# Optimization experiments

Hardware: AMD Instinct MI355X
Metric: run time of the kernel (lower is better)

The kernel has to match this reference:

```python
import jax, jax.numpy as jnp
import numpy as np

B, S, I, H, A = 512, 256, 12, 256, 9


def _lstm_layer(x, w_ih, w_hh, b_ih, b_hh):
    # x: [B,S,in] -> outputs [B,S,H], final (h, c). PyTorch gate order i,f,g,o.
    b, s, _ = x.shape
    h_dim = w_hh.shape[1]
    xg = jnp.einsum('bsi,gi->bsg', x, w_ih) + b_ih  # [B,S,4H] precomputed input gates

    def step(carry, xg_t):
        h, c = carry
        gates = xg_t + h @ w_hh.T + b_hh
        i_g, f_g, g_g, o_g = jnp.split(gates, 4, axis=-1)
        c = jax.nn.sigmoid(f_g) * c + jax.nn.sigmoid(i_g) * jnp.tanh(g_g)
        h = jax.nn.sigmoid(o_g) * jnp.tanh(c)
        return (h, c), h

    init = (jnp.zeros((b, h_dim), x.dtype), jnp.zeros((b, h_dim), x.dtype))
    (h, c), ys = jax.lax.scan(step, init, jnp.swapaxes(xg, 0, 1))
    return jnp.swapaxes(ys, 0, 1), h, c


def setup_inputs() -> dict:
    key = jax.random.key(0)
    ks = jax.random.split(key, 20)
    sc = 0.1
    inp = {
        'x': jax.random.normal(ks[0], (B, S, I), jnp.float32),
        'mask': jnp.ones((B, A), jnp.float32),
        'W_emb': jax.random.normal(ks[1], (H, I), jnp.float32) * sc,
        'b_emb': jnp.zeros((H,), jnp.float32),
        'w_ih0': jax.random.normal(ks[2], (4 * H, H), jnp.float32) * sc,
        'w_hh0': jax.random.normal(ks[3], (4 * H, H), jnp.float32) * sc,
        'b_ih0': jnp.zeros((4 * H,), jnp.float32),
        'b_hh0': jnp.zeros((4 * H,), jnp.float32),
        'w_ih1': jax.random.normal(ks[4], (4 * H, H), jnp.float32) * sc,
        'w_hh1': jax.random.normal(ks[5], (4 * H, H), jnp.float32) * sc,
        'b_ih1': jnp.zeros((4 * H,), jnp.float32),
        'b_hh1': jnp.zeros((4 * H,), jnp.float32),
        'ln_g': jnp.ones((H,), jnp.float32),
        'ln_b': jnp.zeros((H,), jnp.float32),
        'w1': jax.random.normal(ks[6], (32, H), jnp.float32) * sc,
        'b1': jnp.zeros((32,), jnp.float32),
        'w2': jax.random.normal(ks[7], (A, 32), jnp.float32) * sc,
        'b2': jnp.zeros((A,), jnp.float32),
    }
    return inp


def reference(x, mask, W_emb, b_emb, w_ih0, w_hh0, b_ih0, b_hh0,
              w_ih1, w_hh1, b_ih1, b_hh1, ln_g, ln_b, w1, b1, w2, b2):
    # embed + ReLU
    emb = jax.nn.relu(jnp.einsum('bsi,hi->bsh', x, W_emb) + b_emb)  # [B,S,H]
    # 2-layer LSTM (dropout between layers is identity in eval mode)
    y0, h0, c0 = _lstm_layer(emb, w_ih0, w_hh0, b_ih0, b_hh0)
    y1, h1, c1 = _lstm_layer(y0, w_ih1, w_hh1, b_ih1, b_hh1)
    last = y1[:, -1, :]  # [B,H]
    # LayerNorm
    mu = jnp.mean(last, axis=-1, keepdims=True)
    var = jnp.mean((last - mu) ** 2, axis=-1, keepdims=True)
    normed = (last - mu) / jnp.sqrt(var + 1e-5) * ln_g + ln_b
    # MLP head (dropout identity in eval)
    hdn = jax.nn.relu(normed @ w1.T + b1)
    logits = hdn @ w2.T + b2  # [B,A]
    logits = logits + (1.0 - mask) * -1e9
    hidden = (jnp.stack([h0, h1]), jnp.stack([c0, c1]))
    return logits, hidden
```

## Files before the change

### kernel.cpp

```cpp
#include <hip/hip_runtime.h>
#include <cstdint>
#include <cstddef>

typedef __attribute__((ext_vector_type(8))) short short8;
typedef __attribute__((ext_vector_type(4))) float f32x4;

#define MFMA16(a, b, c) __builtin_amdgcn_mfma_f32_16x16x32_bf16((a), (b), (c), 0, 0, 0)

constexpr int kB = 512, kS = 256, kI = 12, kH = 256, kA = 9;
constexpr int kNS = 8;
constexpr int kNB = 32;
constexpr int LDH = 264;
constexpr int LDG = 132;
constexpr int kBH = kB * kH;
constexpr int FLS = 512;

constexpr int OUT_H = kB * kA;
constexpr int OUT_C = OUT_H + 2 * kBH;

__device__ __forceinline__ short f2bf(float f) {
  uint32_t u = __float_as_uint(f);
  u += 0x7fffu + ((u >> 16) & 1u);
  return (short)(u >> 16);
}
__device__ __forceinline__ float fast_sigmoid(float v) {
  return __builtin_amdgcn_rcpf(1.f + __expf(-v));
}
__device__ __forceinline__ float fast_tanh(float v) {
  return 2.f * __builtin_amdgcn_rcpf(1.f + __expf(-2.f * v)) - 1.f;
}

__global__ __launch_bounds__(256, 1) void lstm_scan_kernel(
    const float* __restrict__ x,
    const float* __restrict__ W_emb, const float* __restrict__ b_emb,
    const float* __restrict__ w_ih0, const float* __restrict__ w_hh0,
    const float* __restrict__ b_ih0, const float* __restrict__ b_hh0,
    const float* __restrict__ w_ih1, const float* __restrict__ w_hh1,
    const float* __restrict__ b_ih1, const float* __restrict__ b_hh1,
    unsigned short* __restrict__ h0ex, unsigned short* __restrict__ h1ex,
    int* __restrict__ flags,
    float* __restrict__ dout)
{
  const int tid   = threadIdx.x;
  const int btile = blockIdx.x & (kNB - 1);
  const int slice = blockIdx.x >> 5;
  const int b0    = btile * 16;
  const int lane  = tid & 63;
  const int wave  = tid >> 6;
  const int n16   = lane & 15;
  const int quad  = lane >> 4;

  __shared__ short embL[16 * LDH];
  __shared__ short hA[16 * LDH];
  __shared__ short hB[16 * LDH];
  __shared__ float gL0[16 * LDG];
  __shared__ float gL1[16 * LDG];

  for (int i = tid; i < 16 * LDH; i += 256) { hA[i] = 0; hB[i] = 0; }

  const float* Wm[4] = { w_ih0, w_hh0, w_ih1, w_hh1 };
  short8 wB[2][4][8];
#pragma unroll
  for (int ti = 0; ti < 2; ++ti) {
    const int nt   = wave + ti * 4;
    const int gcol = (nt >> 1) * kH + slice * 32 + (nt & 1) * 16 + n16;
#pragma unroll
    for (int mat = 0; mat < 4; ++mat) {
      const float* wp = Wm[mat] + (size_t)gcol * kH;
#pragma unroll
      for (int kk = 0; kk < 8; ++kk) {
        const float* p = wp + kk * 32 + quad * 8;
        const float4 f0 = *(const float4*)p;
        const float4 f1 = *(const float4*)(p + 4);
        short8 v;
        v[0] = f2bf(f0.x); v[1] = f2bf(f0.y); v[2] = f2bf(f0.z); v[3] = f2bf(f0.w);
        v[4] = f2bf(f1.x); v[5] = f2bf(f1.y); v[6] = f2bf(f1.z); v[7] = f2bf(f1.w);
        wB[ti][mat][kk] = v;
      }
    }
  }
  short8 wE[4];
  float bembv[4];
#pragma unroll
  for (int i = 0; i < 4; ++i) {
    const int col = wave * 64 + i * 16 + n16;
    short8 v;
#pragma unroll
    for (int j = 0; j < 8; ++j) {
      const int k = quad * 8 + j;
      v[j] = (k < kI) ? f2bf(W_emb[col * kI + k]) : (short)0;
    }
    wE[i] = v;
    bembv[i] = b_emb[col];
  }
  const int erow = tid >> 4;
  const int ec   = (tid & 15) * 2;
  float bi0[2][4], bi1[2][4];
#pragma unroll
  for (int j = 0; j < 2; ++j) {
    const int col = slice * 32 + ec + j;
#pragma unroll
    for (int g = 0; g < 4; ++g) {
      bi0[j][g] = b_ih0[g * kH + col] + b_hh0[g * kH + col];
      bi1[j][g] = b_ih1[g * kH + col] + b_hh1[g * kH + col];
    }
  }
  float c0v[2] = {0.f, 0.f}, c1v[2] = {0.f, 0.f};

  {
    const float* xr = x + (size_t)(b0 + n16) * kS * kI;
    short8 xa;
#pragma unroll
    for (int j = 0; j < 8; ++j) {
      const int k = quad * 8 + j;
      xa[j] = (k < kI) ? f2bf(xr[k]) : (short)0;
    }
#pragma unroll
    for (int i = 0; i < 4; ++i) {
      f32x4 z = {0.f, 0.f, 0.f, 0.f};
      f32x4 e = MFMA16(xa, wE[i], z);
      const int col = wave * 64 + i * 16 + n16;
#pragma unroll
      for (int r = 0; r < 4; ++r) {
        float v = e[r] + bembv[i];
        v = v > 0.f ? v : 0.f;
        embL[(quad * 4 + r) * LDH + col] = f2bf(v);
      }
    }
  }
  __syncthreads();

  int* const fl = flags + btile * FLS;

  for (int p = 0; p <= kS; ++p) {
    const int par = p & 1;

    {
      f32x4 a0 = {0.f,0.f,0.f,0.f}, a1 = a0, g1b0 = a0, g1b1 = a0;
#pragma unroll
      for (int kk = 0; kk < 8; ++kk) {
        const short8 ha = *(const short8*)&hA[n16 * LDH + kk * 32 + quad * 8];
        a0   = MFMA16(ha, wB[0][1][kk], a0);
        a1   = MFMA16(ha, wB[1][1][kk], a1);
        g1b0 = MFMA16(ha, wB[0][2][kk], g1b0);
        g1b1 = MFMA16(ha, wB[1][2][kk], g1b1);
      }
#pragma unroll
      for (int kk = 0; kk < 8; ++kk) {
        const short8 e = *(const short8*)&embL[n16 * LDH + kk * 32 + quad * 8];
        a0 = MFMA16(e, wB[0][0][kk], a0);
        a1 = MFMA16(e, wB[1][0][kk], a1);
      }
#pragma unroll
      for (int kk = 0; kk < 8; ++kk) {
        const short8 hb = *(const short8*)&hB[n16 * LDH + kk * 32 + quad * 8];
        g1b0 = MFMA16(hb, wB[0][3][kk], g1b0);
        g1b1 = MFMA16(hb, wB[1][3][kk], g1b1);
      }
#pragma unroll
      for (int ti = 0; ti < 2; ++ti) {
        const int nt = wave + ti * 4;
        const int lcol = (nt >> 1) * 32 + (nt & 1) * 16 + n16;
        const f32x4 va = ti ? a1 : a0;
        const f32x4 vb = ti ? g1b1 : g1b0;
#pragma unroll
        for (int r = 0; r < 4; ++r) {
          gL0[(quad * 4 + r) * LDG + lcol] = va[r];
          gL1[(quad * 4 + r) * LDG + lcol] = vb[r];
        }
      }
    }
    __syncthreads();

    if (p < kS) {
      float hj[2];
#pragma unroll
      for (int j = 0; j < 2; ++j) {
        const int u = ec + j;
        const float iv = gL0[erow * LDG +       u] + bi0[j][0];
        const float fv = gL0[erow * LDG +  32 + u] + bi0[j][1];
        const float gv = gL0[erow * LDG +  64 + u] + bi0[j][2];
        const float ov = gL0[erow * LDG +  96 + u] + bi0[j][3];
        const float c = fast_sigmoid(fv) * c0v[j] + fast_sigmoid(iv) * fast_tanh(gv);
        c0v[j] = c;
        hj[j] = fast_sigmoid(ov) * fast_tanh(c);
      }
      const uint32_t pk = (uint32_t)(uint16_t)f2bf(hj[0]) |
                          ((uint32_t)(uint16_t)f2bf(hj[1]) << 16);
      uint32_t* dst = (uint32_t*)&h0ex[(size_t)par * kBH + (size_t)(b0 + erow) * kH + slice * 32 + ec];
      __hip_atomic_store(dst, pk, __ATOMIC_RELAXED, __HIP_MEMORY_SCOPE_AGENT);
      if (p == kS - 1) {
#pragma unroll
        for (int j = 0; j < 2; ++j) {
          const int col = slice * 32 + ec + j;
          dout[OUT_H + (size_t)(b0 + erow) * kH + col] = hj[j];
          dout[OUT_C + (size_t)(b0 + erow) * kH + col] = c0v[j];
        }
      }
    }
    if (p >= 1) {
      float hj[2];
#pragma unroll
      for (int j = 0; j < 2; ++j) {
        const int u = ec + j;
        const float iv = gL1[erow * LDG +       u] + bi1[j][0];
        const float fv = gL1[erow * LDG +  32 + u] + bi1[j][1];
        const float gv = gL1[erow * LDG +  64 + u] + bi1[j][2];
        const float ov = gL1[erow * LDG +  96 + u] + bi1[j][3];
        const float c = fast_sigmoid(fv) * c1v[j] + fast_sigmoid(iv) * fast_tanh(gv);
        c1v[j] = c;
        hj[j] = fast_sigmoid(ov) * fast_tanh(c);
      }
      const uint32_t pk = (uint32_t)(uint16_t)f2bf(hj[0]) |
                          ((uint32_t)(uint16_t)f2bf(hj[1]) << 16);
      uint32_t* dst = (uint32_t*)&h1ex[(size_t)par * kBH + (size_t)(b0 + erow) * kH + slice * 32 + ec];
      __hip_atomic_store(dst, pk, __ATOMIC_RELAXED, __HIP_MEMORY_SCOPE_AGENT);
      if (p == kS) {
#pragma unroll
        for (int j = 0; j < 2; ++j) {
          const int col = slice * 32 + ec + j;
          dout[OUT_H + kBH + (size_t)(b0 + erow) * kH + col] = hj[j];
          dout[OUT_C + kBH + (size_t)(b0 + erow) * kH + col] = c1v[j];
        }
      }
    }
    __syncthreads();

    if (p < kS) {
      if (tid == 0)
        __hip_atomic_fetch_add(fl + p, 1, __ATOMIC_RELAXED, __HIP_MEMORY_SCOPE_AGENT);

      if (p + 1 < kS) {
        const float* xr = x + ((size_t)(b0 + n16) * kS + (p + 1)) * kI;
        short8 xa;
#pragma unroll
        for (int j = 0; j < 8; ++j) {
          const int k = quad * 8 + j;
          xa[j] = (k < kI) ? f2bf(xr[k]) : (short)0;
        }
#pragma unroll
        for (int i = 0; i < 4; ++i) {
          f32x4 z = {0.f, 0.f, 0.f, 0.f};
          f32x4 e = MFMA16(xa, wE[i], z);
          const int col = wave * 64 + i * 16 + n16;
#pragma unroll
          for (int r = 0; r < 4; ++r) {
            float v = e[r] + bembv[i];
            v = v > 0.f ? v : 0.f;
            embL[(quad * 4 + r) * LDH + col] = f2bf(v);
          }
        }
      }

      while (__hip_atomic_load(fl + p, __ATOMIC_RELAXED, __HIP_MEMORY_SCOPE_AGENT) < kNS)
        __builtin_amdgcn_s_sleep(1);

      {
        const int rr = tid >> 4;
        const int cc = (tid & 15) * 16;
        const size_t base = (size_t)par * kBH + (size_t)(b0 + rr) * kH + cc;
        const uint64_t* s0 = (const uint64_t*)&h0ex[base];
        const uint64_t* s1 = (const uint64_t*)&h1ex[base];
        uint64_t va0 = __hip_atomic_load(s0 + 0, __ATOMIC_RELAXED, __HIP_MEMORY_SCOPE_AGENT);
        uint64_t va1 = __hip_atomic_load(s0 + 1, __ATOMIC_RELAXED, __HIP_MEMORY_SCOPE_AGENT);
        uint64_t va2 = __hip_atomic_load(s0 + 2, __ATOMIC_RELAXED, __HIP_MEMORY_SCOPE_AGENT);
        uint64_t va3 = __hip_atomic_load(s0 + 3, __ATOMIC_RELAXED, __HIP_MEMORY_SCOPE_AGENT);
        uint64_t vb0 = __hip_atomic_load(s1 + 0, __ATOMIC_RELAXED, __HIP_MEMORY_SCOPE_AGENT);
        uint64_t vb1 = __hip_atomic_load(s1 + 1, __ATOMIC_RELAXED, __HIP_MEMORY_SCOPE_AGENT);
        uint64_t vb2 = __hip_atomic_load(s1 + 2, __ATOMIC_RELAXED, __HIP_MEMORY_SCOPE_AGENT);
        uint64_t vb3 = __hip_atomic_load(s1 + 3, __ATOMIC_RELAXED, __HIP_MEMORY_SCOPE_AGENT);
        uint64_t* dA = (uint64_t*)&hA[rr * LDH + cc];
        uint64_t* dB = (uint64_t*)&hB[rr * LDH + cc];
        dA[0] = va0; dA[1] = va1; dA[2] = va2; dA[3] = va3;
        dB[0] = vb0; dB[1] = vb1; dB[2] = vb2; dB[3] = vb3;
      }
      __syncthreads();
    }
  }
}

__global__ __launch_bounds__(64) void head_kernel(
    const float* __restrict__ h1last, const float* __restrict__ mask,
    const float* __restrict__ ln_g, const float* __restrict__ ln_b,
    const float* __restrict__ w1, const float* __restrict__ b1,
    const float* __restrict__ w2, const float* __restrict__ b2,
    float* __restrict__ out)
{
  const int r = blockIdx.x;
  const int lane = threadIdx.x;
  __shared__ float ns[kH];
  __shared__ float hd[32];
  const float4 v = *(const float4*)&h1last[r * kH + lane * 4];
  float vv[4] = {v.x, v.y, v.z, v.w};
  float s = vv[0] + vv[1] + vv[2] + vv[3];
#pragma unroll
  for (int off = 32; off > 0; off >>= 1) s += __shfl_xor(s, off, 64);
  const float mean = s * (1.f / kH);
  float q = 0.f;
#pragma unroll
  for (int j = 0; j < 4; ++j) { const float d = vv[j] - mean; q += d * d; }
#pragma unroll
  for (int off = 32; off > 0; off >>= 1) q += __shfl_xor(q, off, 64);
  const float rstd = rsqrtf(q * (1.f / kH) + 1e-5f);
#pragma unroll
  for (int j = 0; j < 4; ++j) {
    const int c = lane * 4 + j;
    ns[c] = (vv[j] - mean) * rstd * ln_g[c] + ln_b[c];
  }
  __syncthreads();
  if (lane < 32) {
    float a = b1[lane];
    const float* wr = w1 + lane * kH;
    for (int k = 0; k < kH; ++k) a += ns[k] * wr[k];
    hd[lane] = a > 0.f ? a : 0.f;
  }
  __syncthreads();
  if (lane < kA) {
    float a = b2[lane];
    const float* wr = w2 + lane * 32;
#pragma unroll
    for (int k = 0; k < 32; ++k) a += hd[k] * wr[k];
    a += (1.f - mask[r * kA + lane]) * (-1e9f);
    out[r * kA + lane] = a;
  }
}

extern "C" void kernel_launch(void* const* d_in, const int* in_sizes, int n_in,
                              void* d_out, int out_size, void* d_ws, size_t ws_size,
                              hipStream_t stream)
{
  (void)in_sizes; (void)n_in; (void)out_size; (void)ws_size;
  const float* x     = (const float*)d_in[0];
  const float* mask  = (const float*)d_in[1];
  const float* W_emb = (const float*)d_in[2];
  const float* b_emb = (const float*)d_in[3];
  const float* w_ih0 = (const float*)d_in[4];
  const float* w_hh0 = (const float*)d_in[5];
  const float* b_ih0 = (const float*)d_in[6];
  const float* b_hh0 = (const float*)d_in[7];
  const float* w_ih1 = (const float*)d_in[8];
  const float* w_hh1 = (const float*)d_in[9];
  const float* b_ih1 = (const float*)d_in[10];
  const float* b_hh1 = (const float*)d_in[11];
  const float* ln_g  = (const float*)d_in[12];
  const float* ln_b  = (const float*)d_in[13];
  const float* w1    = (const float*)d_in[14];
  const float* b1    = (const float*)d_in[15];
  const float* w2    = (const float*)d_in[16];
  const float* b2    = (const float*)d_in[17];
  float* out = (float*)d_out;

  unsigned short* h0ex = (unsigned short*)d_ws;
  unsigned short* h1ex = h0ex + 2 * kBH;
  int* flags = (int*)(h1ex + 2 * kBH);
  const size_t flag_bytes = (size_t)kNB * FLS * sizeof(int);

  hipMemsetAsync(flags, 0, flag_bytes, stream);
  hipMemsetAsync(h1ex, 0, (size_t)kBH * sizeof(unsigned short), stream);

  lstm_scan_kernel<<<dim3(kNB * kNS), dim3(256), 0, stream>>>(
      x, W_emb, b_emb, w_ih0, w_hh0, b_ih0, b_hh0, w_ih1, w_hh1, b_ih1, b_hh1,
      h0ex, h1ex, flags, out);

  head_kernel<<<dim3(kB), dim3(64), 0, stream>>>(
      out + OUT_H + kBH, mask, ln_g, ln_b, w1, b1, w2, b2, out);
}
```

Baseline: 1.173 ms.

## Double workgroup size so each wave owns one gate tile per step

The recurrent scan kernel goes from 256 to 512 threads per block. Each of the 8 waves now computes one 16-column gate tile instead of two, and each thread updates one hidden unit instead of two. The embedding, gate and exchange-load work is re-split to match. The goal is to shorten the serial MFMA and elementwise chain per timestep and cut per-wave register pressure, at the cost of wider block barriers and narrower 16-bit atomic stores.

```diff
diff --git a/kernel.cpp b/kernel.cpp
--- a/kernel.cpp
+++ b/kernel.cpp
@@ -10,6 +10,7 @@
 constexpr int kB = 512, kS = 256, kI = 12, kH = 256, kA = 9;
 constexpr int kNS = 8;
 constexpr int kNB = 32;
+constexpr int kT  = 512;
 constexpr int LDH = 264;
 constexpr int LDG = 132;
 constexpr int kBH = kB * kH;
@@ -30,7 +31,7 @@
   return 2.f * __builtin_amdgcn_rcpf(1.f + __expf(-2.f * v)) - 1.f;
 }
 
-__global__ __launch_bounds__(256, 1) void lstm_scan_kernel(
+__global__ __launch_bounds__(kT, 2) void lstm_scan_kernel(
     const float* __restrict__ x,
     const float* __restrict__ W_emb, const float* __restrict__ b_emb,
     const float* __restrict__ w_ih0, const float* __restrict__ w_hh0,
@@ -56,14 +57,12 @@
   __shared__ float gL0[16 * LDG];
   __shared__ float gL1[16 * LDG];
 
-  for (int i = tid; i < 16 * LDH; i += 256) { hA[i] = 0; hB[i] = 0; }
+  for (int i = tid; i < 16 * LDH; i += kT) { hA[i] = 0; hB[i] = 0; }
 
   const float* Wm[4] = { w_ih0, w_hh0, w_ih1, w_hh1 };
-  short8 wB[2][4][8];
-#pragma unroll
-  for (int ti = 0; ti < 2; ++ti) {
-    const int nt   = wave + ti * 4;
-    const int gcol = (nt >> 1) * kH + slice * 32 + (nt & 1) * 16 + n16;
+  short8 wB[4][8];
+  {
+    const int gcol = (wave >> 1) * kH + slice * 32 + (wave & 1) * 16 + n16;
 #pragma unroll
     for (int mat = 0; mat < 4; ++mat) {
       const float* wp = Wm[mat] + (size_t)gcol * kH;
@@ -75,15 +74,15 @@
         short8 v;
         v[0] = f2bf(f0.x); v[1] = f2bf(f0.y); v[2] = f2bf(f0.z); v[3] = f2bf(f0.w);
         v[4] = f2bf(f1.x); v[5] = f2bf(f1.y); v[6] = f2bf(f1.z); v[7] = f2bf(f1.w);
-        wB[ti][mat][kk] = v;
-      }
-    }
-  }
-  short8 wE[4];
-  float bembv[4];
-#pragma unroll
-  for (int i = 0; i < 4; ++i) {
-    const int col = wave * 64 + i * 16 + n16;
+        wB[mat][kk] = v;
+      }
+    }
+  }
+  short8 wE[2];
+  float bembv[2];
+#pragma unroll
+  for (int i = 0; i < 2; ++i) {
+    const int col = wave * 32 + i * 16 + n16;
     short8 v;
 #pragma unroll
     for (int j = 0; j < 8; ++j) {
@@ -93,19 +92,16 @@
     wE[i] = v;
     bembv[i] = b_emb[col];
   }
-  const int erow = tid >> 4;
-  const int ec   = (tid & 15) * 2;
-  float bi0[2][4], bi1[2][4];
-#pragma unroll
-  for (int j = 0; j < 2; ++j) {
-    const int col = slice * 32 + ec + j;
-#pragma unroll
-    for (int g = 0; g < 4; ++g) {
-      bi0[j][g] = b_ih0[g * kH + col] + b_hh0[g * kH + col];
-      bi1[j][g] = b_ih1[g * kH + col] + b_hh1[g * kH + col];
-    }
-  }
-  float c0v[2] = {0.f, 0.f}, c1v[2] = {0.f, 0.f};
+  const int erow = tid >> 5;
+  const int ec   = tid & 31;
+  const int ecol = slice * 32 + ec;
+  float bi0[4], bi1[4];
+#pragma unroll
+  for (int g = 0; g < 4; ++g) {
+    bi0[g] = b_ih0[g * kH + ecol] + b_hh0[g * kH + ecol];
+    bi1[g] = b_ih1[g * kH + ecol] + b_hh1[g * kH + ecol];
+  }
+  float c0v = 0.f, c1v = 0.f;
 
   {
     const float* xr = x + (size_t)(b0 + n16) * kS * kI;
@@ -116,10 +112,10 @@
       xa[j] = (k < kI) ? f2bf(xr[k]) : (short)0;
     }
 #pragma unroll
-    for (int i = 0; i < 4; ++i) {
+    for (int i = 0; i < 2; ++i) {
       f32x4 z = {0.f, 0.f, 0.f, 0.f};
       f32x4 e = MFMA16(xa, wE[i], z);
-      const int col = wave * 64 + i * 16 + n16;
+      const int col = wave * 32 + i * 16 + n16;
 #pragma unroll
       for (int r = 0; r < 4; ++r) {
         float v = e[r] + bembv[i];
@@ -136,92 +132,60 @@
     const int par = p & 1;
 
     {
-      f32x4 a0 = {0.f,0.f,0.f,0.f}, a1 = a0, g1b0 = a0, g1b1 = a0;
+      f32x4 a0 = {0.f,0.f,0.f,0.f}, g1 = a0;
 #pragma unroll
       for (int kk = 0; kk < 8; ++kk) {
         const short8 ha = *(const short8*)&hA[n16 * LDH + kk * 32 + quad * 8];
-        a0   = MFMA16(ha, wB[0][1][kk], a0);
-        a1   = MFMA16(ha, wB[1][1][kk], a1);
-        g1b0 = MFMA16(ha, wB[0][2][kk], g1b0);
-        g1b1 = MFMA16(ha, wB[1][2][kk], g1b1);
+        a0 = MFMA16(ha, wB[1][kk], a0);
+        g1 = MFMA16(ha, wB[2][kk], g1);
       }
 #pragma unroll
       for (int kk = 0; kk < 8; ++kk) {
         const short8 e = *(const short8*)&embL[n16 * LDH + kk * 32 + quad * 8];
-        a0 = MFMA16(e, wB[0][0][kk], a0);
-        a1 = MFMA16(e, wB[1][0][kk], a1);
+        a0 = MFMA16(e, wB[0][kk], a0);
       }
 #pragma unroll
       for (int kk = 0; kk < 8; ++kk) {
         const short8 hb = *(const short8*)&hB[n16 * LDH + kk * 32 + quad * 8];
-        g1b0 = MFMA16(hb, wB[0][3][kk], g1b0);
-        g1b1 = MFMA16(hb, wB[1][3][kk], g1b1);
-      }
-#pragma unroll
-      for (int ti = 0; ti < 2; ++ti) {
-        const int nt = wave + ti * 4;
-        const int lcol = (nt >> 1) * 32 + (nt & 1) * 16 + n16;
-        const f32x4 va = ti ? a1 : a0;
-        const f32x4 vb = ti ? g1b1 : g1b0;
-#pragma unroll
-        for (int r = 0; r < 4; ++r) {
-          gL0[(quad * 4 + r) * LDG + lcol] = va[r];
-          gL1[(quad * 4 + r) * LDG + lcol] = vb[r];
-        }
+        g1 = MFMA16(hb, wB[3][kk], g1);
+      }
+      const int lcol = (wave >> 1) * 32 + (wave & 1) * 16 + n16;
+#pragma unroll
+      for (int r = 0; r < 4; ++r) {
+        gL0[(quad * 4 + r) * LDG + lcol] = a0[r];
+        gL1[(quad * 4 + r) * LDG + lcol] = g1[r];
       }
     }
     __syncthreads();
 
     if (p < kS) {
-      float hj[2];
-#pragma unroll
-      for (int j = 0; j < 2; ++j) {
-        const int u = ec + j;
-        const float iv = gL0[erow * LDG +       u] + bi0[j][0];
-        const float fv = gL0[erow * LDG +  32 + u] + bi0[j][1];
-        const float gv = gL0[erow * LDG +  64 + u] + bi0[j][2];
-        const float ov = gL0[erow * LDG +  96 + u] + bi0[j][3];
-        const float c = fast_sigmoid(fv) * c0v[j] + fast_sigmoid(iv) * fast_tanh(gv);
-        c0v[j] = c;
-        hj[j] = fast_sigmoid(ov) * fast_tanh(c);
-      }
-      const uint32_t pk = (uint32_t)(uint16_t)f2bf(hj[0]) |
-                          ((uint32_t)(uint16_t)f2bf(hj[1]) << 16);
-      uint32_t* dst = (uint32_t*)&h0ex[(size_t)par * kBH + (size_t)(b0 + erow) * kH + slice * 32 + ec];
-      __hip_atomic_store(dst, pk, __ATOMIC_RELAXED, __HIP_MEMORY_SCOPE_AGENT);
+      const float iv = gL0[erow * LDG +       ec] + bi0[0];
+      const float fv = gL0[erow * LDG +  32 + ec] + bi0[1];
+      const float gv = gL0[erow * LDG +  64 + ec] + bi0[2];
+      const float ov = gL0[erow * LDG +  96 + ec] + bi0[3];
+      const float c = fast_sigmoid(fv) * c0v + fast_sigmoid(iv) * fast_tanh(gv);
+      c0v = c;
+      const float h = fast_sigmoid(ov) * fast_tanh(c);
+      unsigned short* dst = &h0ex[(size_t)par * kBH + (size_t)(b0 + erow) * kH + ecol];
+      __hip_atomic_store(dst, (unsigned short)f2bf(h), __ATOMIC_RELAXED, __HIP_MEMORY_SCOPE_AGENT);
       if (p == kS - 1) {
-#pragma unroll
-        for (int j = 0; j < 2; ++j) {
-          const int col = slice * 32 + ec + j;
-          dout[OUT_H + (size_t)(b0 + erow) * kH + col] = hj[j];
-          dout[OUT_C + (size_t)(b0 + erow) * kH + col] = c0v[j];
-        }
+        dout[OUT_H + (size_t)(b0 + erow) * kH + ecol] = h;
+        dout[OUT_C + (size_t)(b0 + erow) * kH + ecol] = c;
       }
     }
     if (p >= 1) {
-      float hj[2];
-#pragma unroll
-      for (int j = 0; j < 2; ++j) {
-        const int u = ec + j;
-        const float iv = gL1[erow * LDG +       u] + bi1[j][0];
-        const float fv = gL1[erow * LDG +  32 + u] + bi1[j][1];
-        const float gv = gL1[erow * LDG +  64 + u] + bi1[j][2];
-        const float ov = gL1[erow * LDG +  96 + u] + bi1[j][3];
-        const float c = fast_sigmoid(fv) * c1v[j] + fast_sigmoid(iv) * fast_tanh(gv);
-        c1v[j] = c;
-        hj[j] = fast_sigmoid(ov) * fast_tanh(c);
-      }
-      const uint32_t pk = (uint32_t)(uint16_t)f2bf(hj[0]) |
-                          ((uint32_t)(uint16_t)f2bf(hj[1]) << 16);
-      uint32_t* dst = (uint32_t*)&h1ex[(size_t)par * kBH + (size_t)(b0 + erow) * kH + slice * 32 + ec];
-      __hip_atomic_store(dst, pk, __ATOMIC_RELAXED, __HIP_MEMORY_SCOPE_AGENT);
+      const float iv = gL1[erow * LDG +       ec] + bi1[0];
+      const float fv = gL1[erow * LDG +  32 + ec] + bi1[1];
+      const float gv = gL1[erow * LDG +  64 + ec] + bi1[2];
+      const float ov = gL1[erow * LDG +  96 + ec] + bi1[3];
+      const float c = fast_sigmoid(fv) * c1v + fast_sigmoid(iv) * fast_tanh(gv);
+      c1v = c;
+      const float h = fast_sigmoid(ov) * fast_tanh(c);
+      unsigned short* dst = &h1ex[(size_t)par * kBH + (size_t)(b0 + erow) * kH + ecol];
+      __hip_atomic_store(dst, (unsigned short)f2bf(h), __ATOMIC_RELAXED, __HIP_MEMORY_SCOPE_AGENT);
       if (p == kS) {
-#pragma unroll
-        for (int j = 0; j < 2; ++j) {
-          const int col = slice * 32 + ec + j;
-          dout[OUT_H + kBH + (size_t)(b0 + erow) * kH + col] = hj[j];
-          dout[OUT_C + kBH + (size_t)(b0 + erow) * kH + col] = c1v[j];
-        }
+        dout[OUT_H + kBH + (size_t)(b0 + erow) * kH + ecol] = h;
+        dout[OUT_C + kBH + (size_t)(b0 + erow) * kH + ecol] = c;
       }
     }
     __syncthreads();
@@ -239,10 +203,10 @@
           xa[j] = (k < kI) ? f2bf(xr[k]) : (short)0;
         }
 #pragma unroll
-        for (int i = 0; i < 4; ++i) {
+        for (int i = 0; i < 2; ++i) {
           f32x4 z = {0.f, 0.f, 0.f, 0.f};
           f32x4 e = MFMA16(xa, wE[i], z);
-          const int col = wave * 64 + i * 16 + n16;
+          const int col = wave * 32 + i * 16 + n16;
 #pragma unroll
           for (int r = 0; r < 4; ++r) {
             float v = e[r] + bembv[i];
@@ -256,23 +220,19 @@
         __builtin_amdgcn_s_sleep(1);
 
       {
-        const int rr = tid >> 4;
-        const int cc = (tid & 15) * 16;
+        const int rr = tid >> 5;
+        const int cc = (tid & 31) * 8;
         const size_t base = (size_t)par * kBH + (size_t)(b0 + rr) * kH + cc;
         const uint64_t* s0 = (const uint64_t*)&h0ex[base];
         const uint64_t* s1 = (const uint64_t*)&h1ex[base];
         uint64_t va0 = __hip_atomic_load(s0 + 0, __ATOMIC_RELAXED, __HIP_MEMORY_SCOPE_AGENT);
         uint64_t va1 = __hip_atomic_load(s0 + 1, __ATOMIC_RELAXED, __HIP_MEMORY_SCOPE_AGENT);
-        uint64_t va2 = __hip_atomic_load(s0 + 2, __ATOMIC_RELAXED, __HIP_MEMORY_SCOPE_AGENT);
-        uint64_t va3 = __hip_atomic_load(s0 + 3, __ATOMIC_RELAXED, __HIP_MEMORY_SCOPE_AGENT);
         uint64_t vb0 = __hip_atomic_load(s1 + 0, __ATOMIC_RELAXED, __HIP_MEMORY_SCOPE_AGENT);
         uint64_t vb1 = __hip_atomic_load(s1 + 1, __ATOMIC_RELAXED, __HIP_MEMORY_SCOPE_AGENT);
-        uint64_t vb2 = __hip_atomic_load(s1 + 2, __ATOMIC_RELAXED, __HIP_MEMORY_SCOPE_AGENT);
-        uint64_t vb3 = __hip_atomic_load(s1 + 3, __ATOMIC_RELAXED, __HIP_MEMORY_SCOPE_AGENT);
         uint64_t* dA = (uint64_t*)&hA[rr * LDH + cc];
         uint64_t* dB = (uint64_t*)&hB[rr * LDH + cc];
-        dA[0] = va0; dA[1] = va1; dA[2] = va2; dA[3] = va3;
-        dB[0] = vb0; dB[1] = vb1; dB[2] = vb2; dB[3] = vb3;
+        dA[0] = va0; dA[1] = va1;
+        dB[0] = vb0; dB[1] = vb1;
       }
       __syncthreads();
     }
@@ -358,7 +318,7 @@
   hipMemsetAsync(flags, 0, flag_bytes, stream);
   hipMemsetAsync(h1ex, 0, (size_t)kBH * sizeof(unsigned short), stream);
 
-  lstm_scan_kernel<<<dim3(kNB * kNS), dim3(256), 0, stream>>>(
+  lstm_scan_kernel<<<dim3(kNB * kNS), dim3(kT), 0, stream>>>(
       x, W_emb, b_emb, w_ih0, w_hh0, b_ih0, b_hh0, w_ih1, w_hh1, b_ih1, b_hh1,
       h0ex, h1ex, flags, out);
 
```

New measurement: 1.012 ms. -13.8%, faster.
